# Kernel optimization log

Hardware: AMD Instinct MI355X
Metric: run time of the kernel (lower is better)

Reference implementation:

```python
import jax, jax.numpy as jnp
import numpy as np
import math

B, S, HID, NH = 2, 2048, 1024, 16
HD = HID // NH


def setup_inputs() -> dict:
    key = jax.random.key(0)
    ks = jax.random.split(key, 6)
    scale = 0.02
    return {
        "hidden_states": jax.random.normal(ks[0], (B, S, HID), dtype=jnp.float32),
        "attention_mask": jnp.ones((B, S), dtype=jnp.float32),
        "Wq": jax.random.normal(ks[1], (HID, HID), dtype=jnp.float32) * scale,
        "bq": jnp.zeros((HID,), dtype=jnp.float32),
        "Wk": jax.random.normal(ks[2], (HID, HID), dtype=jnp.float32) * scale,
        "bk": jnp.zeros((HID,), dtype=jnp.float32),
        "Wv": jax.random.normal(ks[3], (HID, HID), dtype=jnp.float32) * scale,
        "bv": jnp.zeros((HID,), dtype=jnp.float32),
        "Wo": jax.random.normal(ks[4], (HID, HID), dtype=jnp.float32) * scale,
        "bo": jnp.zeros((HID,), dtype=jnp.float32),
        "beta": jnp.zeros((1,), dtype=jnp.float32),
        "gamma": jnp.ones((1,), dtype=jnp.float32),
    }


def reference(hidden_states, attention_mask, Wq, bq, Wk, bk, Wv, bv, Wo, bo, beta, gamma):
    b, s, h = hidden_states.shape

    def proj(W, bias):
        # torch Linear: x @ W.T + b ; then split heads -> [B, NH, S, HD]
        y = jnp.einsum('bsh,oh->bso', hidden_states, W) + bias
        return y.reshape(b, s, NH, HD).transpose(0, 2, 1, 3)

    q = proj(Wq, bq)
    k = proj(Wk, bk)
    v = proj(Wv, bv)

    scores = jnp.einsum('bnsd,bntd->bnst', q, k) / math.sqrt(HD)  # [B,NH,S,S]
    # extended mask: [B,1,1,S]; additive -1e4 on masked positions
    scores = scores + (1.0 - attention_mask)[:, None, None, :] * (-10000.0)

    # ConsMax: exp(scores - beta - rowmax) / gamma (no sum normalization)
    shifted = scores - beta
    shifted = shifted - jnp.max(shifted, axis=-1, keepdims=True)
    probs = jnp.exp(shifted) / gamma  # dropout p=0 -> identity

    ctx = jnp.einsum('bnst,bntd->bnsd', probs, v)  # [B,NH,S,HD]
    ctx = ctx.transpose(0, 2, 1, 3).reshape(b, s, h)
    return jnp.einsum('bsh,oh->bso', ctx, Wo) + bo
```

## Files before the change

### kernel.cpp

```cpp
#include <hip/hip_runtime.h>
#include <hip/hip_bf16.h>


typedef unsigned short u16;
typedef __attribute__((ext_vector_type(8))) short short8;
typedef __attribute__((ext_vector_type(4))) float floatx4;
typedef __attribute__((ext_vector_type(16))) float floatx16;

constexpr int B_  = 2;
constexpr int S_  = 2048;
constexpr int HID = 1024;
constexpr int NH  = 16;
constexpr int HD  = 64;

constexpr float LOG2E   = 1.4426950408889634f;
constexpr float QSCALE  = 0.125f * LOG2E;
constexpr float MSCALE  = -10000.0f * LOG2E;

#if __has_builtin(__builtin_amdgcn_exp2f)
#define EXP2(x) __builtin_amdgcn_exp2f(x)
#else
#define EXP2(x) exp2f(x)
#endif

__device__ __forceinline__ u16 f2us(float f) {
    union { float f; unsigned int i; } x;
    x.f = f;
    unsigned int r = x.i + 0x7FFFu + ((x.i >> 16) & 1u);
    return (u16)(r >> 16);
}
__device__ __forceinline__ unsigned pk2(float a, float b) {
    __hip_bfloat162 h = __float22bfloat162_rn(make_float2(a, b));
    unsigned u; __builtin_memcpy(&u, &h, 4); return u;
}
__device__ __forceinline__ void async_lds16(const u16* g, u16* l) {
    __builtin_amdgcn_global_load_lds(
        (const __attribute__((address_space(1))) unsigned int*)g,
        (__attribute__((address_space(3))) unsigned int*)l, 16, 0, 0);
}

__global__ __launch_bounds__(256)
void cvt_all(const float* __restrict__ hs, const float* __restrict__ Wq,
             const float* __restrict__ Wk, const float* __restrict__ Wv,
             const float* __restrict__ Wo,
             u16* __restrict__ hs_bf, u16* __restrict__ Wcat,
             u16* __restrict__ Wo_bf)
{
    const int bid = blockIdx.x;
    const float* src;
    u16* dst;
    size_t base;
    if (bid < 4096) {
        src = hs; dst = hs_bf; base = (size_t)bid * 1024;
    } else if (bid < 7168) {
        const int s = (bid - 4096) >> 10;
        src = (s == 0) ? Wq : (s == 1) ? Wk : Wv;
        dst = Wcat + (size_t)s * 1048576;
        base = (size_t)((bid - 4096) & 1023) * 1024;
    } else {
        src = Wo; dst = Wo_bf; base = (size_t)(bid - 7168) * 1024;
    }
    const size_t i = base + threadIdx.x * 4;
    float4 t = *(const float4*)(src + i);
    uint2 o = { pk2(t.x, t.y), pk2(t.z, t.w) };
    *(uint2*)(dst + i) = o;
}

__global__ __launch_bounds__(256)
void qkv_gemm(const u16* __restrict__ hs_bf, const u16* __restrict__ Wcat,
              const float* __restrict__ bq, const float* __restrict__ bk,
              const float* __restrict__ bv,
              u16* __restrict__ Qo, u16* __restrict__ Ko, u16* __restrict__ VT)
{
    __shared__ u16 Alds[3][4096];
    __shared__ u16 Blds[3][4096];

    const int tid = threadIdx.x;
    const int id  = blockIdx.x;
    const int xcd = id & 7, jb = id >> 3;
    const int m0  = (xcd * 4 + (jb & 3)) * 128;
    const int n0g = (jb >> 2) * 128;
    const int p   = n0g >> 10;
    const int n0  = n0g & 1023;
    const u16*   Wb = Wcat + (size_t)p * 1048576;
    const float* bi = (p == 0) ? bq : (p == 1) ? bk : bv;
    const float  osc = (p == 0) ? QSCALE : 1.0f;

    const int w = tid >> 6, l = tid & 63;
    const int quad = l >> 4, l16 = l & 15;
    const int wy = w >> 1, wx = w & 1;

    floatx4 acc[4][4];
    #pragma unroll
    for (int i = 0; i < 4; ++i)
        #pragma unroll
        for (int j = 0; j < 4; ++j) acc[i][j] = (floatx4){0.f, 0.f, 0.f, 0.f};

    auto stage = [&](int ks, int bf) {
        const int k0 = ks * 32;
        #pragma unroll
        for (int c = 0; c < 2; ++c) {
            const int s = w * 2 + c;
            async_lds16(hs_bf + (size_t)(m0 + s * 16 + l16) * HID + k0 + quad * 8,
                        &Alds[bf][s * 512]);
            async_lds16(Wb + (size_t)(n0 + s * 16 + l16) * HID + k0 + quad * 8,
                        &Blds[bf][s * 512]);
        }
    };

    constexpr int NS = HID / 32;
    stage(0, 0);
    stage(1, 1);

    for (int ks = 0; ks < NS; ++ks) {
        const int cur = ks % 3;
        if (ks < NS - 1) asm volatile("s_waitcnt vmcnt(4)" ::: "memory");
        else             asm volatile("s_waitcnt vmcnt(0)" ::: "memory");
        __builtin_amdgcn_s_barrier();
        if (ks + 2 < NS) stage(ks + 2, (ks + 2) % 3);

        short8 afr[4], bfr[4];
        #pragma unroll
        for (int i = 0; i < 4; ++i)
            afr[i] = *(const short8*)&Alds[cur][(wy * 4 + i) * 512 + l * 8];
        #pragma unroll
        for (int j = 0; j < 4; ++j)
            bfr[j] = *(const short8*)&Blds[cur][(wx * 4 + j) * 512 + l * 8];
        #pragma unroll
        for (int i = 0; i < 4; ++i)
            #pragma unroll
            for (int j = 0; j < 4; ++j)
                acc[i][j] = __builtin_amdgcn_mfma_f32_16x16x32_bf16(afr[i], bfr[j], acc[i][j], 0, 0, 0);
    }

    #pragma unroll
    for (int i = 0; i < 4; ++i)
        #pragma unroll
        for (int j = 0; j < 4; ++j) {
            const int nn   = n0 + wx * 64 + j * 16 + l16;
            const int head = nn >> 6, dd = nn & 63;
            const float bb_ = bi[nn];
            const int mmb = m0 + wy * 64 + i * 16 + quad * 4;
            const int b = mmb >> 11, ss = mmb & (S_ - 1);
            if (p == 2) {
                uint2 st = { pk2(acc[i][j][0] + bb_, acc[i][j][1] + bb_),
                             pk2(acc[i][j][2] + bb_, acc[i][j][3] + bb_) };
                *(uint2*)(VT + (((size_t)(b * NH + head)) * HD + dd) * S_ + ss) = st;
            } else {
                u16* Out = (p == 0) ? Qo : Ko;
                #pragma unroll
                for (int rg = 0; rg < 4; ++rg)
                    Out[(((size_t)b * NH + head) * S_ + ss + rg) * HD + dd] =
                        f2us((acc[i][j][rg] + bb_) * osc);
            }
        }
}

__global__ __launch_bounds__(256, 2)
void attn12(const u16* __restrict__ Qg, const u16* __restrict__ Kg,
            const u16* __restrict__ VTg, const float* __restrict__ mask,
            const float* __restrict__ gamma, u16* __restrict__ ctx)
{
    __shared__ u16 Kb[3][4096];
    __shared__ u16 Vb[3][4096];
    __shared__ u16 Pq[8192];
    __shared__ float Mb[2048];

    const int tid = threadIdx.x;
    const int w = tid >> 6, l = tid & 63;
    const int l32 = l & 31, hh = l >> 5;
    const int swz = (l32 & 7) << 3;
    const int id  = blockIdx.x;
    const int xcd = id & 7, jb = id >> 3;
    const int bh  = xcd * 4 + (jb >> 4);
    const int qb  = jb & 15;
    const int b0  = bh >> 4, h = bh & (NH - 1);

    const u16* Qb    = Qg  + (size_t)bh * S_ * HD;
    const u16* Kbg   = Kg  + (size_t)bh * S_ * HD;
    const u16* Vbg   = VTg + (size_t)bh * HD * S_;
    const float* mG  = mask + (size_t)b0 * S_;

    const int qrow = qb * 128 + w * 32 + l32;

    short8 qB[4];
    #pragma unroll
    for (int dc = 0; dc < 4; ++dc)
        qB[dc] = *(const short8*)(Qb + (size_t)qrow * HD + dc * 16 + hh * 8);

    {
        float4 ma = *(const float4*)(mG + tid * 8);
        float4 mb2 = *(const float4*)(mG + tid * 8 + 4);
        float* d = &Mb[tid * 8];
        d[0] = fmaf(ma.x, -MSCALE, MSCALE);
        d[1] = fmaf(ma.y, -MSCALE, MSCALE);
        d[2] = fmaf(ma.z, -MSCALE, MSCALE);
        d[3] = fmaf(ma.w, -MSCALE, MSCALE);
        d[4] = fmaf(mb2.x, -MSCALE, MSCALE);
        d[5] = fmaf(mb2.y, -MSCALE, MSCALE);
        d[6] = fmaf(mb2.z, -MSCALE, MSCALE);
        d[7] = fmaf(mb2.w, -MSCALE, MSCALE);
    }

    floatx16 oacc[2];
    #pragma unroll
    for (int db = 0; db < 2; ++db)
        #pragma unroll
        for (int i = 0; i < 16; ++i) oacc[db][i] = 0.f;
    float m_run = -1e30f;

    u16* Pw = Pq + w * 2048;

    auto stage = [&](int kt, int bf) {
        #pragma unroll
        for (int c = 0; c < 2; ++c) {
            const int r = w * 2 + c;
            const int kb = r >> 2, dc = r & 3;
            async_lds16(Kbg + (size_t)(kt * 64 + kb * 32 + l32) * HD + dc * 16 + hh * 8,
                        &Kb[bf][r * 512]);
            const int db = r >> 2, kg = r & 3;
            async_lds16(Vbg + (size_t)(db * 32 + l32) * S_ + kt * 64 + kg * 16 + hh * 8,
                        &Vb[bf][r * 512]);
        }
    };

    __syncthreads();
    constexpr int NT = S_ / 64;
    stage(0, 0);
    stage(1, 1);

    for (int kt = 0; kt < NT; ++kt) {
        const int cur = kt % 3;
        if (kt < NT - 1) asm volatile("s_waitcnt vmcnt(4)" ::: "memory");
        else             asm volatile("s_waitcnt vmcnt(0)" ::: "memory");
        __builtin_amdgcn_s_barrier();
        if (kt + 2 < NT) stage(kt + 2, (kt + 2) % 3);

        #pragma unroll
        for (int kb = 0; kb < 2; ++kb) {
            const float* mrow = &Mb[kt * 64 + kb * 32 + 4 * hh];
            floatx16 acc;
            #pragma unroll
            for (int g = 0; g < 4; ++g) {
                float4 mv = *(const float4*)(mrow + g * 8);
                acc[4*g]   = mv.x;
                acc[4*g+1] = mv.y;
                acc[4*g+2] = mv.z;
                acc[4*g+3] = mv.w;
            }
            #pragma unroll
            for (int dc = 0; dc < 4; ++dc) {
                short8 kf = *(const short8*)&Kb[cur][(kb * 4 + dc) * 512 + l * 8];
                acc = __builtin_amdgcn_mfma_f32_32x32x16_bf16(kf, qB[dc], acc, 0, 0, 0);
            }
            float mr = m_run;
            #pragma unroll
            for (int i = 0; i < 16; ++i) mr = fmaxf(mr, acc[i]);
            m_run = mr;
            #pragma unroll
            for (int g = 0; g < 4; ++g) {
                uint2 pw = { pk2(EXP2(acc[4*g]),   EXP2(acc[4*g+1])),
                             pk2(EXP2(acc[4*g+2]), EXP2(acc[4*g+3])) };
                const int koff = kb * 32 + 8 * g + 4 * hh;
                *(uint2*)&Pw[l32 * 64 + (koff ^ swz)] = pw;
            }
        }

        #pragma unroll
        for (int kg = 0; kg < 4; ++kg) {
            short8 pf = *(const short8*)&Pw[l32 * 64 + ((kg * 16 + hh * 8) ^ swz)];
            #pragma unroll
            for (int db = 0; db < 2; ++db) {
                short8 vf = *(const short8*)&Vb[cur][(db * 4 + kg) * 512 + l * 8];
                oacc[db] = __builtin_amdgcn_mfma_f32_32x32x16_bf16(vf, pf, oacc[db], 0, 0, 0);
            }
        }
    }

    const float mx = fmaxf(m_run, __shfl_xor(m_run, 32, 64));
    const float si = EXP2(-mx) * (1.0f / gamma[0]);
    u16* crow = ctx + (size_t)(b0 * S_ + qrow) * HID + h * HD;
    #pragma unroll
    for (int db = 0; db < 2; ++db)
        #pragma unroll
        for (int g = 0; g < 4; ++g) {
            uint2 st = { pk2(oacc[db][g * 4 + 0] * si, oacc[db][g * 4 + 1] * si),
                         pk2(oacc[db][g * 4 + 2] * si, oacc[db][g * 4 + 3] * si) };
            *(uint2*)(crow + db * 32 + g * 8 + hh * 4) = st;
        }
}

__global__ __launch_bounds__(256)
void out_gemm(const u16* __restrict__ ctx, const u16* __restrict__ Wo_bf,
              const float* __restrict__ bo, float* __restrict__ out)
{
    __shared__ u16 Alds[3][4096];
    __shared__ u16 Blds[3][2048];

    const int tid = threadIdx.x;
    const int id  = blockIdx.x;
    const int xcd = id & 7, jb = id >> 3;
    const int m0  = (xcd * 4 + (jb & 3)) * 128;
    const int n0  = (jb >> 2) * 64;

    const int w = tid >> 6, l = tid & 63;
    const int quad = l >> 4, l16 = l & 15;

    floatx4 acc[2][4];
    #pragma unroll
    for (int i = 0; i < 2; ++i)
        #pragma unroll
        for (int j = 0; j < 4; ++j) acc[i][j] = (floatx4){0.f, 0.f, 0.f, 0.f};

    auto stage = [&](int ks, int bf) {
        const int k0 = ks * 32;
        #pragma unroll
        for (int c = 0; c < 2; ++c) {
            const int s = w * 2 + c;
            async_lds16(ctx + (size_t)(m0 + s * 16 + l16) * HID + k0 + quad * 8,
                        &Alds[bf][s * 512]);
        }
        async_lds16(Wo_bf + (size_t)(n0 + w * 16 + l16) * HID + k0 + quad * 8,
                    &Blds[bf][w * 512]);
    };

    constexpr int NS = HID / 32;
    stage(0, 0);
    stage(1, 1);

    for (int ks = 0; ks < NS; ++ks) {
        const int cur = ks % 3;
        if (ks < NS - 1) asm volatile("s_waitcnt vmcnt(3)" ::: "memory");
        else             asm volatile("s_waitcnt vmcnt(0)" ::: "memory");
        __builtin_amdgcn_s_barrier();
        if (ks + 2 < NS) stage(ks + 2, (ks + 2) % 3);

        short8 afr[2], bfr[4];
        #pragma unroll
        for (int i = 0; i < 2; ++i)
            afr[i] = *(const short8*)&Alds[cur][(w * 2 + i) * 512 + l * 8];
        #pragma unroll
        for (int j = 0; j < 4; ++j)
            bfr[j] = *(const short8*)&Blds[cur][j * 512 + l * 8];
        #pragma unroll
        for (int i = 0; i < 2; ++i)
            #pragma unroll
            for (int j = 0; j < 4; ++j)
                acc[i][j] = __builtin_amdgcn_mfma_f32_16x16x32_bf16(afr[i], bfr[j], acc[i][j], 0, 0, 0);
    }

    #pragma unroll
    for (int i = 0; i < 2; ++i)
        #pragma unroll
        for (int j = 0; j < 4; ++j) {
            const int nn = n0 + j * 16 + l16;
            const float bb_ = bo[nn];
            #pragma unroll
            for (int rg = 0; rg < 4; ++rg) {
                const int mm = m0 + w * 32 + i * 16 + quad * 4 + rg;
                out[(size_t)mm * HID + nn] = acc[i][j][rg] + bb_;
            }
        }
}

extern "C" void kernel_launch(void* const* d_in, const int* in_sizes, int n_in,
                              void* d_out, int out_size, void* d_ws, size_t ws_size,
                              hipStream_t stream)
{
    const float* hs    = (const float*)d_in[0];
    const float* mask  = (const float*)d_in[1];
    const float* Wq    = (const float*)d_in[2];
    const float* bq    = (const float*)d_in[3];
    const float* Wk    = (const float*)d_in[4];
    const float* bk    = (const float*)d_in[5];
    const float* Wv    = (const float*)d_in[6];
    const float* bv    = (const float*)d_in[7];
    const float* Wo    = (const float*)d_in[8];
    const float* bo    = (const float*)d_in[9];
    const float* gamma = (const float*)d_in[11];
    float* out = (float*)d_out;

    const size_t tsz = (size_t)B_ * NH * S_ * HD;
    u16* q     = (u16*)d_ws;
    u16* vT    = q + tsz;
    u16* Wcat  = vT + tsz;
    u16* Wo_bf = Wcat + 3u * 1048576u;
    u16* ctx   = Wo_bf + 1048576u;
    u16* hs_bf = (u16*)d_out;
    u16* kbuf  = hs_bf + tsz;

    cvt_all<<<dim3(8192), 256, 0, stream>>>(hs, Wq, Wk, Wv, Wo, hs_bf, Wcat, Wo_bf);
    qkv_gemm<<<dim3(768), 256, 0, stream>>>(hs_bf, Wcat, bq, bk, bv, q, kbuf, vT);
    attn12<<<dim3(512), 256, 0, stream>>>(q, kbuf, vT, mask, gamma, ctx);
    out_gemm<<<dim3(512), 256, 0, stream>>>(ctx, Wo_bf, bo, out);
}
```

Before: 238.9 us.

## Split attention KV loop across two wave groups per block with LDS reduction

The attention kernel now launches 512 threads per block: four wave pairs each handle the same 32 query rows, and the two waves of a pair take alternate 32-key tiles. Each wave keeps its own running max and output accumulator, and the two halves are merged through shared memory at the end. This doubles the waves per block to raise latency hiding and MFMA occupancy, at the cost of an extra LDS reduction, two added barriers and a larger register/LDS footprint under launch_bounds(512,4). Merging without rescaling is still correct because the kernel exponentiates raw scores and only applies exp(-max) in the final scaling step.

```diff
diff --git a/kernel.cpp b/kernel.cpp
--- a/kernel.cpp
+++ b/kernel.cpp
@@ -156,20 +156,22 @@
         }
 }
 
-__global__ __launch_bounds__(256, 2)
-void attn12(const u16* __restrict__ Qg, const u16* __restrict__ Kg,
+__global__ __launch_bounds__(512, 4)
+void attn13(const u16* __restrict__ Qg, const u16* __restrict__ Kg,
             const u16* __restrict__ VTg, const float* __restrict__ mask,
             const float* __restrict__ gamma, u16* __restrict__ ctx)
 {
-    __shared__ u16 Kb[3][4096];
-    __shared__ u16 Vb[3][4096];
-    __shared__ u16 Pq[8192];
-    __shared__ float Mb[2048];
+    __shared__ u16 SMEM[36864];
+    u16*   KbB = SMEM;
+    u16*   VbB = SMEM + 12288;
+    u16*   PqB = SMEM + 24576;
+    float* Mb  = (float*)(SMEM + 32768);
 
     const int tid = threadIdx.x;
     const int w = tid >> 6, l = tid & 63;
+    const int wq = w & 3, wk = w >> 2;
     const int l32 = l & 31, hh = l >> 5;
-    const int swz = (l32 & 7) << 3;
+    const int swz = (l32 & 3) << 3;
     const int id  = blockIdx.x;
     const int xcd = id & 7, jb = id >> 3;
     const int bh  = xcd * 4 + (jb >> 4);
@@ -181,7 +183,7 @@
     const u16* Vbg   = VTg + (size_t)bh * HD * S_;
     const float* mG  = mask + (size_t)b0 * S_;
 
-    const int qrow = qb * 128 + w * 32 + l32;
+    const int qrow = qb * 128 + wq * 32 + l32;
 
     short8 qB[4];
     #pragma unroll
@@ -189,17 +191,12 @@
         qB[dc] = *(const short8*)(Qb + (size_t)qrow * HD + dc * 16 + hh * 8);
 
     {
-        float4 ma = *(const float4*)(mG + tid * 8);
-        float4 mb2 = *(const float4*)(mG + tid * 8 + 4);
-        float* d = &Mb[tid * 8];
-        d[0] = fmaf(ma.x, -MSCALE, MSCALE);
-        d[1] = fmaf(ma.y, -MSCALE, MSCALE);
-        d[2] = fmaf(ma.z, -MSCALE, MSCALE);
-        d[3] = fmaf(ma.w, -MSCALE, MSCALE);
-        d[4] = fmaf(mb2.x, -MSCALE, MSCALE);
-        d[5] = fmaf(mb2.y, -MSCALE, MSCALE);
-        d[6] = fmaf(mb2.z, -MSCALE, MSCALE);
-        d[7] = fmaf(mb2.w, -MSCALE, MSCALE);
+        float4 mv = *(const float4*)(mG + tid * 4);
+        float* d = &Mb[tid * 4];
+        d[0] = fmaf(mv.x, -MSCALE, MSCALE);
+        d[1] = fmaf(mv.y, -MSCALE, MSCALE);
+        d[2] = fmaf(mv.z, -MSCALE, MSCALE);
+        d[3] = fmaf(mv.w, -MSCALE, MSCALE);
     }
 
     floatx16 oacc[2];
@@ -209,85 +206,102 @@
         for (int i = 0; i < 16; ++i) oacc[db][i] = 0.f;
     float m_run = -1e30f;
 
-    u16* Pw = Pq + w * 2048;
-
-    auto stage = [&](int kt, int bf) {
-        #pragma unroll
-        for (int c = 0; c < 2; ++c) {
-            const int r = w * 2 + c;
-            const int kb = r >> 2, dc = r & 3;
-            async_lds16(Kbg + (size_t)(kt * 64 + kb * 32 + l32) * HD + dc * 16 + hh * 8,
-                        &Kb[bf][r * 512]);
-            const int db = r >> 2, kg = r & 3;
-            async_lds16(Vbg + (size_t)(db * 32 + l32) * S_ + kt * 64 + kg * 16 + hh * 8,
-                        &Vb[bf][r * 512]);
-        }
+    u16* Kbuf = KbB + wk * 6144;
+    u16* Vbuf = VbB + wk * 6144;
+    u16* Pw   = PqB + w * 1024;
+
+    auto stage = [&](int i, int bf) {
+        const int kt = 2 * i + wk;
+        async_lds16(Kbg + (size_t)(kt * 32 + l32) * HD + wq * 16 + hh * 8,
+                    Kbuf + bf * 2048 + wq * 512);
+        const int db = wq >> 1, kg = wq & 1;
+        async_lds16(Vbg + (size_t)(db * 32 + l32) * S_ + kt * 32 + kg * 16 + hh * 8,
+                    Vbuf + bf * 2048 + wq * 512);
     };
 
     __syncthreads();
-    constexpr int NT = S_ / 64;
+    constexpr int NI = 32;
     stage(0, 0);
     stage(1, 1);
 
-    for (int kt = 0; kt < NT; ++kt) {
-        const int cur = kt % 3;
-        if (kt < NT - 1) asm volatile("s_waitcnt vmcnt(4)" ::: "memory");
-        else             asm volatile("s_waitcnt vmcnt(0)" ::: "memory");
+    for (int i = 0; i < NI; ++i) {
+        const int cur = i % 3;
+        if (i < NI - 1) asm volatile("s_waitcnt vmcnt(2)" ::: "memory");
+        else            asm volatile("s_waitcnt vmcnt(0)" ::: "memory");
         __builtin_amdgcn_s_barrier();
-        if (kt + 2 < NT) stage(kt + 2, (kt + 2) % 3);
-
-        #pragma unroll
-        for (int kb = 0; kb < 2; ++kb) {
-            const float* mrow = &Mb[kt * 64 + kb * 32 + 4 * hh];
-            floatx16 acc;
-            #pragma unroll
-            for (int g = 0; g < 4; ++g) {
-                float4 mv = *(const float4*)(mrow + g * 8);
-                acc[4*g]   = mv.x;
-                acc[4*g+1] = mv.y;
-                acc[4*g+2] = mv.z;
-                acc[4*g+3] = mv.w;
-            }
-            #pragma unroll
-            for (int dc = 0; dc < 4; ++dc) {
-                short8 kf = *(const short8*)&Kb[cur][(kb * 4 + dc) * 512 + l * 8];
-                acc = __builtin_amdgcn_mfma_f32_32x32x16_bf16(kf, qB[dc], acc, 0, 0, 0);
-            }
-            float mr = m_run;
-            #pragma unroll
-            for (int i = 0; i < 16; ++i) mr = fmaxf(mr, acc[i]);
-            m_run = mr;
-            #pragma unroll
-            for (int g = 0; g < 4; ++g) {
-                uint2 pw = { pk2(EXP2(acc[4*g]),   EXP2(acc[4*g+1])),
-                             pk2(EXP2(acc[4*g+2]), EXP2(acc[4*g+3])) };
-                const int koff = kb * 32 + 8 * g + 4 * hh;
-                *(uint2*)&Pw[l32 * 64 + (koff ^ swz)] = pw;
-            }
-        }
-
-        #pragma unroll
-        for (int kg = 0; kg < 4; ++kg) {
-            short8 pf = *(const short8*)&Pw[l32 * 64 + ((kg * 16 + hh * 8) ^ swz)];
+        if (i + 2 < NI) stage(i + 2, (i + 2) % 3);
+
+        const int kt = 2 * i + wk;
+
+        const float* mrow = &Mb[kt * 32 + 4 * hh];
+        floatx16 acc;
+        #pragma unroll
+        for (int g = 0; g < 4; ++g) {
+            float4 mv = *(const float4*)(mrow + g * 8);
+            acc[4*g]   = mv.x;
+            acc[4*g+1] = mv.y;
+            acc[4*g+2] = mv.z;
+            acc[4*g+3] = mv.w;
+        }
+        #pragma unroll
+        for (int dc = 0; dc < 4; ++dc) {
+            short8 kf = *(const short8*)&Kbuf[cur * 2048 + dc * 512 + l * 8];
+            acc = __builtin_amdgcn_mfma_f32_32x32x16_bf16(kf, qB[dc], acc, 0, 0, 0);
+        }
+
+        float mr = m_run;
+        #pragma unroll
+        for (int ii = 0; ii < 16; ++ii) mr = fmaxf(mr, acc[ii]);
+        m_run = mr;
+        #pragma unroll
+        for (int g = 0; g < 4; ++g) {
+            uint2 pw = { pk2(EXP2(acc[4*g]),   EXP2(acc[4*g+1])),
+                         pk2(EXP2(acc[4*g+2]), EXP2(acc[4*g+3])) };
+            const int koff = 8 * g + 4 * hh;
+            *(uint2*)&Pw[l32 * 32 + (koff ^ swz)] = pw;
+        }
+
+        #pragma unroll
+        for (int kg = 0; kg < 2; ++kg) {
+            short8 pf = *(const short8*)&Pw[l32 * 32 + ((kg * 16 + hh * 8) ^ swz)];
             #pragma unroll
             for (int db = 0; db < 2; ++db) {
-                short8 vf = *(const short8*)&Vb[cur][(db * 4 + kg) * 512 + l * 8];
+                short8 vf = *(const short8*)&Vbuf[cur * 2048 + (db * 2 + kg) * 512 + l * 8];
                 oacc[db] = __builtin_amdgcn_mfma_f32_32x32x16_bf16(vf, pf, oacc[db], 0, 0, 0);
             }
         }
     }
 
-    const float mx = fmaxf(m_run, __shfl_xor(m_run, 32, 64));
-    const float si = EXP2(-mx) * (1.0f / gamma[0]);
-    u16* crow = ctx + (size_t)(b0 * S_ + qrow) * HID + h * HD;
-    #pragma unroll
-    for (int db = 0; db < 2; ++db)
-        #pragma unroll
-        for (int g = 0; g < 4; ++g) {
-            uint2 st = { pk2(oacc[db][g * 4 + 0] * si, oacc[db][g * 4 + 1] * si),
-                         pk2(oacc[db][g * 4 + 2] * si, oacc[db][g * 4 + 3] * si) };
-            *(uint2*)(crow + db * 32 + g * 8 + hh * 4) = st;
-        }
+    __syncthreads();
+    float* OS = (float*)SMEM;
+    if (wk == 1) {
+        float* d = OS + (size_t)(wq * 64 + l) * 33;
+        #pragma unroll
+        for (int db = 0; db < 2; ++db)
+            #pragma unroll
+            for (int ii = 0; ii < 16; ++ii) d[db * 16 + ii] = oacc[db][ii];
+        d[32] = m_run;
+    }
+    __syncthreads();
+    if (wk == 0) {
+        const float* s = OS + (size_t)(wq * 64 + l) * 33;
+        #pragma unroll
+        for (int db = 0; db < 2; ++db)
+            #pragma unroll
+            for (int ii = 0; ii < 16; ++ii) oacc[db][ii] += s[db * 16 + ii];
+        m_run = fmaxf(m_run, s[32]);
+        const float mx = fmaxf(m_run, __shfl_xor(m_run, 32, 64));
+        const float si = EXP2(-mx) * (1.0f / gamma[0]);
+        u16* crow = ctx + (size_t)(b0 * S_ + qrow) * HID + h * HD;
+        #pragma unroll
+        for (int db = 0; db < 2; ++db)
+            #pragma unroll
+            for (int g = 0; g < 4; ++g) {
+                uint2 st = { pk2(oacc[db][g * 4 + 0] * si, oacc[db][g * 4 + 1] * si),
+                             pk2(oacc[db][g * 4 + 2] * si, oacc[db][g * 4 + 3] * si) };
+                *(uint2*)(crow + db * 32 + g * 8 + hh * 4) = st;
+            }
+    }
 }
 
 __global__ __launch_bounds__(256)
@@ -391,6 +405,6 @@
 
     cvt_all<<<dim3(8192), 256, 0, stream>>>(hs, Wq, Wk, Wv, Wo, hs_bf, Wcat, Wo_bf);
     qkv_gemm<<<dim3(768), 256, 0, stream>>>(hs_bf, Wcat, bq, bk, bv, q, kbuf, vT);
-    attn12<<<dim3(512), 256, 0, stream>>>(q, kbuf, vT, mask, gamma, ctx);
+    attn13<<<dim3(512), 512, 0, stream>>>(q, kbuf, vT, mask, gamma, ctx);
     out_gemm<<<dim3(512), 256, 0, stream>>>(ctx, Wo_bf, bo, out);
 }
```

Result: faster. 233.9 us (-2.1%).
